# Kernel optimization log

Hardware: AMD Instinct MI355X
Metric: run time of the kernel (lower is better)

## Reference

```python
import jax, jax.numpy as jnp
import numpy as np

N_NODES = 100000
D_IN = 128
H_DIM = 128
N_EDGES = 1600000


def _gcn_conv(x, src, dst, dinv, W, b):
    # PyG GCNConv(improved=True): h = x @ W; out = A_hat h + b,
    # A_hat = D^{-1/2} (A + 2I) D^{-1/2}
    h = x @ W                                   # [N, H]
    norm = dinv[src] * dinv[dst]                # [E]
    agg = jnp.zeros_like(h).at[dst].add(h[src] * norm[:, None])
    agg = agg + h * (2.0 * dinv * dinv)[:, None]  # self-loop, weight 2.0
    return agg + b


def setup_inputs() -> dict:
    key = jax.random.key(0)
    ks = jax.random.split(key, 12)
    s = 1.0 / np.sqrt(D_IN)
    sh = 1.0 / np.sqrt(2 * H_DIM)
    inp = {
        "x": jax.random.normal(ks[0], (N_NODES, D_IN), jnp.float32),
        "edge_index": jax.random.randint(ks[1], (2, N_EDGES), 0, N_NODES, jnp.int64),
        # GCNConv weights (in -> hidden), bias
        "Wz": jax.random.uniform(ks[2], (D_IN, H_DIM), jnp.float32, -s, s),
        "bz": jnp.zeros((H_DIM,), jnp.float32),
        "Wr": jax.random.uniform(ks[3], (D_IN, H_DIM), jnp.float32, -s, s),
        "br": jnp.zeros((H_DIM,), jnp.float32),
        "Wh": jax.random.uniform(ks[4], (D_IN, H_DIM), jnp.float32, -s, s),
        "bh": jnp.zeros((H_DIM,), jnp.float32),
        # TGCN gate linears: Linear(2h, h)
        "lzW": jax.random.uniform(ks[5], (2 * H_DIM, H_DIM), jnp.float32, -sh, sh),
        "lzb": jax.random.uniform(ks[6], (H_DIM,), jnp.float32, -sh, sh),
        "lrW": jax.random.uniform(ks[7], (2 * H_DIM, H_DIM), jnp.float32, -sh, sh),
        "lrb": jax.random.uniform(ks[8], (H_DIM,), jnp.float32, -sh, sh),
        "lhW": jax.random.uniform(ks[9], (2 * H_DIM, H_DIM), jnp.float32, -sh, sh),
        "lhb": jax.random.uniform(ks[10], (H_DIM,), jnp.float32, -sh, sh),
        # final linear2: hidden -> 1
        "W2": jax.random.uniform(ks[11], (H_DIM, 1), jnp.float32, -1 / np.sqrt(H_DIM), 1 / np.sqrt(H_DIM)),
        "b2": jnp.zeros((1,), jnp.float32),
    }
    return inp


def reference(x, edge_index, Wz, bz, Wr, br, Wh, bh, lzW, lzb, lrW, lrb, lhW, lhb, W2, b2):
    src, dst = edge_index[0], edge_index[1]
    n = x.shape[0]
    # improved GCN norm: deg includes self-loop weight 2
    deg = jnp.zeros((n,), x.dtype).at[dst].add(jnp.ones_like(src, x.dtype)) + 2.0
    dinv = jnp.where(deg > 0, deg ** -0.5, 0.0)
    # TGCN cell with H0 = 0
    H0 = jnp.zeros((n, Wz.shape[1]), x.dtype)
    Z = jax.nn.sigmoid(jnp.concatenate([_gcn_conv(x, src, dst, dinv, Wz, bz), H0], axis=1) @ lzW + lzb)
    R = jax.nn.sigmoid(jnp.concatenate([_gcn_conv(x, src, dst, dinv, Wr, br), H0], axis=1) @ lrW + lrb)
    Ht = jnp.tanh(jnp.concatenate([_gcn_conv(x, src, dst, dinv, Wh, bh), H0 * R], axis=1) @ lhW + lhb)
    H = Z * H0 + (1.0 - Z) * Ht
    # forward: relu output is discarded (y = h overwrites), then linear2
    return H @ W2 + b2
```

## Files before the change

### kernel.cpp

```cpp
#include <hip/hip_runtime.h>
#include <math.h>

#define D 128
#define BSHIFT 9
#define CAP 12288
#define EPT 13
#define P1B 481
#define XCB 12500

typedef __attribute__((ext_vector_type(8))) short s8v;
typedef __attribute__((ext_vector_type(8))) unsigned short us8;
typedef __attribute__((ext_vector_type(4))) unsigned short us4;
typedef __attribute__((ext_vector_type(4))) float f4v;

__device__ __forceinline__ float bf2f(unsigned short u) {
    union { unsigned int i; float f; } v; v.i = ((unsigned int)u) << 16; return v.f;
}
__device__ __forceinline__ unsigned short f2bf(float f) {
    union { float f; unsigned int i; } v; v.f = f;
    unsigned int r = v.i + 0x7FFFu + ((v.i >> 16) & 1u);
    return (unsigned short)(r >> 16);
}

__global__ __launch_bounds__(256) void k_combo(
    const int* __restrict__ src, const int* __restrict__ dst, int E,
    int* __restrict__ bcur, unsigned int* __restrict__ pairs,
    const float* __restrict__ x, unsigned short* __restrict__ xb, int n4,
    const float* __restrict__ Wz, const float* __restrict__ bz,
    const float* __restrict__ lzW, const float* __restrict__ lzb,
    const float* __restrict__ Wh, const float* __restrict__ bh,
    const float* __restrict__ lhW, const float* __restrict__ lhb,
    unsigned short* __restrict__ Mt, float* __restrict__ c) {
    __shared__ int cnt[256];
    __shared__ int base[256];
    int bx = blockIdx.x, tid = threadIdx.x;

    if (bx < P1B) {
        unsigned int pk[EPT]; int rkbk[EPT];
        int e0 = bx * (EPT * 256) + tid;
        cnt[tid] = 0;
        __syncthreads();
        #pragma unroll
        for (int i = 0; i < EPT; ++i) {
            int e = e0 + i * 256;
            bool ok = e < E;
            int d = ok ? dst[e] : 0;
            int s = ok ? src[e] : 0;
            int bk = d >> BSHIFT;
            pk[i] = ((unsigned int)(d & ((1 << BSHIFT) - 1)) << 17) | (unsigned int)s;
            int r = ok ? atomicAdd(&cnt[bk], 1) : 0;
            rkbk[i] = (bk << 16) | r;
        }
        __syncthreads();
        if (cnt[tid] > 0) base[tid] = tid * CAP + atomicAdd(&bcur[tid], cnt[tid]);
        __syncthreads();
        #pragma unroll
        for (int i = 0; i < EPT; ++i) {
            int e = e0 + i * 256;
            if (e < E) {
                int bk = rkbk[i] >> 16;
                pairs[base[bk] + (rkbk[i] & 0xffff)] = pk[i];
            }
        }
    } else if (bx < P1B + XCB) {
        int i = (bx - P1B) * 256 + tid;
        if (i < n4) {
            float4 v = ((const float4*)x)[i];
            us4 o;
            o[0] = f2bf(v.x); o[1] = f2bf(v.y); o[2] = f2bf(v.z); o[3] = f2bf(v.w);
            ((us4*)xb)[i] = o;
        }
    } else {
        int k = bx - (P1B + XCB);
        int j = tid;
        int jj = j & 127;
        const float* W = (j < 128) ? Wz : Wh;
        const float* L = (j < 128) ? lzW : lhW;
        float s = 0.f;
        for (int t = 0; t < 128; ++t) s += W[k * 128 + t] * L[t * 128 + jj];
        Mt[(size_t)j * 128 + k] = f2bf(s);
        if (k == 0) {
            const float* b  = (j < 128) ? bz  : bh;
            const float* lb = (j < 128) ? lzb : lhb;
            float cs = lb[jj];
            for (int t = 0; t < 128; ++t) cs += b[t] * L[t * 128 + jj];
            c[j] = cs;
        }
    }
}

__global__ __launch_bounds__(256) void k_part2(const unsigned int* __restrict__ pairs,
                                               const int* __restrict__ bcur,
                                               int NB, int N, int E,
                                               int* __restrict__ rowptr,
                                               float* __restrict__ dinv,
                                               int* __restrict__ esrc) {
    __shared__ int cnt[512];
    __shared__ int lcur[512];
    __shared__ int ts[256];
    int b = blockIdx.x, tid = threadIdx.x;
    int n0 = b << BSHIFT;
    int nn = min(N - n0, 1 << BSHIFT);
    int tot = bcur[b];
    long pbase = (long)b * CAP;

    ts[tid] = (tid < b) ? bcur[tid] : 0;
    __syncthreads();
    for (int off = 128; off > 0; off >>= 1) {
        if (tid < off) ts[tid] += ts[tid + off];
        __syncthreads();
    }
    int obase = ts[0];
    __syncthreads();

    cnt[tid] = 0; cnt[tid + 256] = 0;
    __syncthreads();
    for (int i = tid; i < tot; i += 256)
        atomicAdd(&cnt[pairs[pbase + i] >> 17], 1);
    __syncthreads();

    int a0 = cnt[2 * tid], a1 = cnt[2 * tid + 1];
    int s = a0 + a1;
    ts[tid] = s; __syncthreads();
    for (int off = 1; off < 256; off <<= 1) {
        int add = (tid >= off) ? ts[tid - off] : 0;
        __syncthreads();
        ts[tid] += add;
        __syncthreads();
    }
    int excl = ts[tid] - s;
    lcur[2 * tid]     = obase + excl;
    lcur[2 * tid + 1] = obase + excl + a0;
    if (2 * tid < nn) {
        rowptr[n0 + 2 * tid] = obase + excl;
        dinv[n0 + 2 * tid]   = rsqrtf((float)a0 + 2.0f);
    }
    if (2 * tid + 1 < nn) {
        rowptr[n0 + 2 * tid + 1] = obase + excl + a0;
        dinv[n0 + 2 * tid + 1]   = rsqrtf((float)a1 + 2.0f);
    }
    if (b == 0 && tid == 0) rowptr[N] = E;
    __syncthreads();

    for (int i = tid; i < tot; i += 256) {
        unsigned int p = pairs[pbase + i];
        int dl = p >> 17;
        int pos = atomicAdd(&lcur[dl], 1);
        esrc[pos] = (int)(p & 0x1FFFFu);
    }
}

__global__ __launch_bounds__(256) void k_gather(const unsigned short* __restrict__ xb,
                                                const int* __restrict__ esrc,
                                                const int* __restrict__ rowptr,
                                                const float* __restrict__ dinv,
                                                unsigned short* __restrict__ xab, int N) {
    int node = (blockIdx.x * blockDim.x + threadIdx.x) >> 5;
    int sub  = threadIdx.x & 31;
    if (node >= N) return;
    int eo = sub >> 4, cs = sub & 15;
    int start = rowptr[node], end = rowptr[node + 1];
    float dd = dinv[node];
    float acc[8];
    #pragma unroll
    for (int j = 0; j < 8; ++j) acc[j] = 0.f;

    for (int base = start; base < end; base += 32) {
        int cnt = min(32, end - base);
        int myedge = 0; float mynorm = 0.f;
        if (sub < cnt) { myedge = esrc[base + sub]; mynorm = dinv[myedge]; }
        int pairs = (cnt + 1) >> 1;
        int i = 0;
        for (; i + 3 < pairs; i += 4) {
            int i0 = 2 * i + eo;
            int   s0 = __shfl(myedge, i0,     32); float w0 = __shfl(mynorm, i0,     32);
            int   s1 = __shfl(myedge, i0 + 2, 32); float w1 = __shfl(mynorm, i0 + 2, 32);
            int   s2 = __shfl(myedge, i0 + 4, 32); float w2 = __shfl(mynorm, i0 + 4, 32);
            int   s3 = __shfl(myedge, i0 + 6, 32); float w3 = __shfl(mynorm, i0 + 6, 32);
            us8 v0 = *(const us8*)(xb + (size_t)s0 * D + cs * 8);
            us8 v1 = *(const us8*)(xb + (size_t)s1 * D + cs * 8);
            us8 v2 = *(const us8*)(xb + (size_t)s2 * D + cs * 8);
            us8 v3 = *(const us8*)(xb + (size_t)s3 * D + cs * 8);
            #pragma unroll
            for (int j = 0; j < 8; ++j) acc[j] += bf2f(v0[j]) * w0;
            #pragma unroll
            for (int j = 0; j < 8; ++j) acc[j] += bf2f(v1[j]) * w1;
            #pragma unroll
            for (int j = 0; j < 8; ++j) acc[j] += bf2f(v2[j]) * w2;
            #pragma unroll
            for (int j = 0; j < 8; ++j) acc[j] += bf2f(v3[j]) * w3;
        }
        for (; i < pairs; ++i) {
            int i0 = 2 * i + eo;
            int   s0 = __shfl(myedge, i0, 32); float w0 = __shfl(mynorm, i0, 32);
            us8 v0 = *(const us8*)(xb + (size_t)s0 * D + cs * 8);
            #pragma unroll
            for (int j = 0; j < 8; ++j) acc[j] += bf2f(v0[j]) * w0;
        }
    }
    #pragma unroll
    for (int j = 0; j < 8; ++j) acc[j] += __shfl_xor(acc[j], 16);
    if (eo == 0) {
        us8 xs = *(const us8*)(xb + (size_t)node * D + cs * 8);
        float sfac = 2.f * dd * dd;
        us8 r;
        #pragma unroll
        for (int j = 0; j < 8; ++j) r[j] = f2bf(acc[j] * dd + bf2f(xs[j]) * sfac);
        *(us8*)(xab + (size_t)node * D + cs * 8) = r;
    }
}

#define ASTRIDE 136
__global__ __launch_bounds__(256, 4) void k_ep_mfma(
    const unsigned short* __restrict__ xab, const unsigned short* __restrict__ Mt,
    const float* __restrict__ c, const float* __restrict__ W2,
    const float* __restrict__ b2, float* __restrict__ out, int N) {
    __shared__ unsigned short Ast[64 * ASTRIDE];
    __shared__ float pbuf[4][64];

    int tid = threadIdx.x;
    int n0 = blockIdx.x * 64;
    int wv = tid >> 6;
    int lane = tid & 63;
    int l = lane & 15, q = lane >> 4;

    #pragma unroll
    for (int j = 0; j < 4; ++j) {
        int idx = tid + 256 * j;
        int row = idx >> 4, c16 = idx & 15;
        us8 v = {0, 0, 0, 0, 0, 0, 0, 0};
        if (n0 + row < N) v = *(const us8*)(xab + (size_t)(n0 + row) * D + c16 * 8);
        *(us8*)&Ast[row * ASTRIDE + c16 * 8] = v;
    }
    __syncthreads();

    int tz0 = 2 * wv;
    f4v acc[4][4];
    #pragma unroll
    for (int i = 0; i < 4; ++i)
        #pragma unroll
        for (int nt = 0; nt < 4; ++nt) acc[i][nt] = (f4v){0.f, 0.f, 0.f, 0.f};

    const unsigned short* Bb = Mt + (size_t)l * 128 + q * 8;

    #pragma unroll
    for (int ks = 0; ks < 4; ++ks) {
        s8v b[4];
        #pragma unroll
        for (int i = 0; i < 2; ++i) {
            b[i]     = *(const s8v*)(Bb + (size_t)(tz0 + i) * 16 * 128 + ks * 32);
            b[2 + i] = *(const s8v*)(Bb + (size_t)(8 + tz0 + i) * 16 * 128 + ks * 32);
        }
        #pragma unroll
        for (int nt = 0; nt < 4; ++nt) {
            s8v a = *(const s8v*)&Ast[(nt * 16 + l) * ASTRIDE + ks * 32 + q * 8];
            #pragma unroll
            for (int i = 0; i < 4; ++i)
                acc[i][nt] = __builtin_amdgcn_mfma_f32_16x16x32_bf16(a, b[i], acc[i][nt], 0, 0, 0);
        }
    }

    float p[4][4];
    #pragma unroll
    for (int nt = 0; nt < 4; ++nt)
        #pragma unroll
        for (int r = 0; r < 4; ++r) p[nt][r] = 0.f;
    #pragma unroll
    for (int i = 0; i < 2; ++i) {
        int col = (tz0 + i) * 16 + l;
        float cz = c[col], ch = c[128 + col], w2 = W2[col];
        #pragma unroll
        for (int nt = 0; nt < 4; ++nt)
            #pragma unroll
            for (int r = 0; r < 4; ++r) {
                float gz = acc[i][nt][r] + cz;
                float gh = acc[2 + i][nt][r] + ch;
                float z  = 1.f / (1.f + __expf(-gz));
                float ht = 1.f - 2.f / (__expf(2.f * gh) + 1.f);
                p[nt][r] += (1.f - z) * ht * w2;
            }
    }
    #pragma unroll
    for (int nt = 0; nt < 4; ++nt)
        #pragma unroll
        for (int r = 0; r < 4; ++r) {
            p[nt][r] += __shfl_xor(p[nt][r], 1);
            p[nt][r] += __shfl_xor(p[nt][r], 2);
            p[nt][r] += __shfl_xor(p[nt][r], 4);
            p[nt][r] += __shfl_xor(p[nt][r], 8);
        }
    if (l == 0) {
        #pragma unroll
        for (int nt = 0; nt < 4; ++nt)
            #pragma unroll
            for (int r = 0; r < 4; ++r)
                pbuf[wv][nt * 16 + q * 4 + r] = p[nt][r];
    }
    __syncthreads();
    if (tid < 64) {
        int n = n0 + tid;
        if (n < N)
            out[n] = pbuf[0][tid] + pbuf[1][tid] + pbuf[2][tid] + pbuf[3][tid] + b2[0];
    }
}

extern "C" void kernel_launch(void* const* d_in, const int* in_sizes, int n_in,
                              void* d_out, int out_size, void* d_ws, size_t ws_size,
                              hipStream_t stream) {
    const float* x    = (const float*)d_in[0];
    const int*   eidx = (const int*)d_in[1];
    const float* Wz   = (const float*)d_in[2];
    const float* bz   = (const float*)d_in[3];
    const float* Wh   = (const float*)d_in[6];
    const float* bh   = (const float*)d_in[7];
    const float* lzW  = (const float*)d_in[8];
    const float* lzb  = (const float*)d_in[9];
    const float* lhW  = (const float*)d_in[12];
    const float* lhb  = (const float*)d_in[13];
    const float* W2   = (const float*)d_in[14];
    const float* b2   = (const float*)d_in[15];
    float* out = (float*)d_out;

    int N = in_sizes[0] / D;
    int E = in_sizes[1] / 2;
    const int* src = eidx;
    const int* dst = eidx + E;
    int NB = (N + (1 << BSHIFT) - 1) >> BSHIFT;

    char* ws = (char*)d_ws;
    size_t off = 0;
    auto alloc = [&](size_t bytes) { void* p = ws + off; off += (bytes + 511) & ~(size_t)511; return p; };
    unsigned short* xb  = (unsigned short*)alloc((size_t)N * D * 2);
    unsigned short* xab = (unsigned short*)alloc((size_t)N * D * 2);
    int*   rowptr = (int*)  alloc((size_t)(N + 1) * 4);
    float* dinv   = (float*)alloc((size_t)N * 4);
    int*   esrc   = (int*)  alloc((size_t)E * 4);
    int*   bcur   = (int*)  alloc(256 * 4);
    unsigned short* Mt = (unsigned short*)alloc(256 * 128 * 2);
    float* c      = (float*)alloc(256 * 4);
    unsigned int* pairs = (unsigned int*)xab;

    hipMemsetAsync(bcur, 0, 256 * sizeof(int), stream);

    int n4 = N * (D / 4);
    k_combo<<<P1B + XCB + 128, 256, 0, stream>>>(
        src, dst, E, bcur, pairs, x, xb, n4,
        Wz, bz, lzW, lzb, Wh, bh, lhW, lhb, Mt, c);
    k_part2<<<NB, 256, 0, stream>>>(pairs, bcur, NB, N, E, rowptr, dinv, esrc);
    k_gather<<<(N * 32 + 255) / 256, 256, 0, stream>>>(xb, esrc, rowptr, dinv, xab, N);
    k_ep_mfma<<<(N + 63) / 64, 256, 0, stream>>>(xab, Mt, c, W2, b2, out, N);
}
```

Baseline: 251.6 us.

## Regroup preprocessing: bucket scatter alone, co-launch CSR build with conversion and weight fold

Edge bucketing now runs as a standalone kernel with 1024-thread blocks. The per-bucket CSR build, the x-to-bf16 conversion and the fused weight-matrix precompute are merged into a second kernel, also using 1024-thread blocks. This lets the bandwidth-heavy x conversion overlap the atomic-heavy CSR construction instead of the edge scatter. It also makes each bucket's block wider, in exchange for more idle threads in the scan phases and heavier shared-memory atomic contention per block.

```diff
diff --git a/kernel.cpp b/kernel.cpp
--- a/kernel.cpp
+++ b/kernel.cpp
@@ -4,9 +4,11 @@
 #define D 128
 #define BSHIFT 9
 #define CAP 12288
-#define EPT 13
-#define P1B 481
-#define XCB 12500
+#define EPT 7
+#define P1B 241
+#define P2B 196
+#define XCB2 3125
+#define PRB 32
 
 typedef __attribute__((ext_vector_type(8))) short s8v;
 typedef __attribute__((ext_vector_type(8))) unsigned short us8;
@@ -22,48 +24,117 @@
     return (unsigned short)(r >> 16);
 }
 
-__global__ __launch_bounds__(256) void k_combo(
+__global__ __launch_bounds__(1024) void k_part1(
     const int* __restrict__ src, const int* __restrict__ dst, int E,
-    int* __restrict__ bcur, unsigned int* __restrict__ pairs,
+    int* __restrict__ bcur, unsigned int* __restrict__ pairs) {
+    __shared__ int cnt[256];
+    __shared__ int base[256];
+    int bx = blockIdx.x, tid = threadIdx.x;
+
+    unsigned int pk[EPT]; int rkbk[EPT];
+    int e0 = bx * (EPT * 1024) + tid;
+    if (tid < 256) cnt[tid] = 0;
+    __syncthreads();
+    #pragma unroll
+    for (int i = 0; i < EPT; ++i) {
+        int e = e0 + i * 1024;
+        bool ok = e < E;
+        int d = ok ? dst[e] : 0;
+        int s = ok ? src[e] : 0;
+        int bk = d >> BSHIFT;
+        pk[i] = ((unsigned int)(d & ((1 << BSHIFT) - 1)) << 17) | (unsigned int)s;
+        int r = ok ? atomicAdd(&cnt[bk], 1) : 0;
+        rkbk[i] = (bk << 16) | r;
+    }
+    __syncthreads();
+    if (tid < 256 && cnt[tid] > 0)
+        base[tid] = tid * CAP + atomicAdd(&bcur[tid], cnt[tid]);
+    __syncthreads();
+    #pragma unroll
+    for (int i = 0; i < EPT; ++i) {
+        int e = e0 + i * 1024;
+        if (e < E) {
+            int bk = rkbk[i] >> 16;
+            pairs[base[bk] + (rkbk[i] & 0xffff)] = pk[i];
+        }
+    }
+}
+
+__global__ __launch_bounds__(1024) void k_mid(
+    const unsigned int* __restrict__ pairs, const int* __restrict__ bcur,
+    int N, int E,
+    int* __restrict__ rowptr, float* __restrict__ dinv, int* __restrict__ esrc,
     const float* __restrict__ x, unsigned short* __restrict__ xb, int n4,
     const float* __restrict__ Wz, const float* __restrict__ bz,
     const float* __restrict__ lzW, const float* __restrict__ lzb,
     const float* __restrict__ Wh, const float* __restrict__ bh,
     const float* __restrict__ lhW, const float* __restrict__ lhb,
     unsigned short* __restrict__ Mt, float* __restrict__ c) {
-    __shared__ int cnt[256];
-    __shared__ int base[256];
     int bx = blockIdx.x, tid = threadIdx.x;
 
-    if (bx < P1B) {
-        unsigned int pk[EPT]; int rkbk[EPT];
-        int e0 = bx * (EPT * 256) + tid;
-        cnt[tid] = 0;
-        __syncthreads();
-        #pragma unroll
-        for (int i = 0; i < EPT; ++i) {
-            int e = e0 + i * 256;
-            bool ok = e < E;
-            int d = ok ? dst[e] : 0;
-            int s = ok ? src[e] : 0;
-            int bk = d >> BSHIFT;
-            pk[i] = ((unsigned int)(d & ((1 << BSHIFT) - 1)) << 17) | (unsigned int)s;
-            int r = ok ? atomicAdd(&cnt[bk], 1) : 0;
-            rkbk[i] = (bk << 16) | r;
-        }
-        __syncthreads();
-        if (cnt[tid] > 0) base[tid] = tid * CAP + atomicAdd(&bcur[tid], cnt[tid]);
-        __syncthreads();
-        #pragma unroll
-        for (int i = 0; i < EPT; ++i) {
-            int e = e0 + i * 256;
-            if (e < E) {
-                int bk = rkbk[i] >> 16;
-                pairs[base[bk] + (rkbk[i] & 0xffff)] = pk[i];
+    if (bx < P2B) {
+        __shared__ int cnt[512];
+        __shared__ int lcur[512];
+        __shared__ int ts[256];
+        int b = bx;
+        int n0 = b << BSHIFT;
+        int nn = min(N - n0, 1 << BSHIFT);
+        int tot = bcur[b];
+        long pbase = (long)b * CAP;
+
+        if (tid < 256) ts[tid] = (tid < b) ? bcur[tid] : 0;
+        __syncthreads();
+        for (int off = 128; off > 0; off >>= 1) {
+            if (tid < off) ts[tid] += ts[tid + off];
+            __syncthreads();
+        }
+        int obase = ts[0];
+        __syncthreads();
+
+        if (tid < 512) cnt[tid] = 0;
+        __syncthreads();
+        for (int i = tid; i < tot; i += 1024)
+            atomicAdd(&cnt[pairs[pbase + i] >> 17], 1);
+        __syncthreads();
+
+        int a0 = 0, a1 = 0, s = 0;
+        if (tid < 256) {
+            a0 = cnt[2 * tid]; a1 = cnt[2 * tid + 1];
+            s = a0 + a1;
+            ts[tid] = s;
+        }
+        __syncthreads();
+        for (int off = 1; off < 256; off <<= 1) {
+            int add = 0;
+            if (tid < 256 && tid >= off) add = ts[tid - off];
+            __syncthreads();
+            if (tid < 256) ts[tid] += add;
+            __syncthreads();
+        }
+        if (tid < 256) {
+            int excl = ts[tid] - s;
+            lcur[2 * tid]     = obase + excl;
+            lcur[2 * tid + 1] = obase + excl + a0;
+            if (2 * tid < nn) {
+                rowptr[n0 + 2 * tid] = obase + excl;
+                dinv[n0 + 2 * tid]   = rsqrtf((float)a0 + 2.0f);
             }
-        }
-    } else if (bx < P1B + XCB) {
-        int i = (bx - P1B) * 256 + tid;
+            if (2 * tid + 1 < nn) {
+                rowptr[n0 + 2 * tid + 1] = obase + excl + a0;
+                dinv[n0 + 2 * tid + 1]   = rsqrtf((float)a1 + 2.0f);
+            }
+            if (b == 0 && tid == 0) rowptr[N] = E;
+        }
+        __syncthreads();
+
+        for (int i = tid; i < tot; i += 1024) {
+            unsigned int p = pairs[pbase + i];
+            int dl = p >> 17;
+            int pos = atomicAdd(&lcur[dl], 1);
+            esrc[pos] = (int)(p & 0x1FFFFu);
+        }
+    } else if (bx < P2B + XCB2) {
+        int i = (bx - P2B) * 1024 + tid;
         if (i < n4) {
             float4 v = ((const float4*)x)[i];
             us4 o;
@@ -71,8 +142,8 @@
             ((us4*)xb)[i] = o;
         }
     } else {
-        int k = bx - (P1B + XCB);
-        int j = tid;
+        int k = (bx - (P2B + XCB2)) * 4 + (tid >> 8);
+        int j = tid & 255;
         int jj = j & 127;
         const float* W = (j < 128) ? Wz : Wh;
         const float* L = (j < 128) ? lzW : lhW;
@@ -86,67 +157,6 @@
             for (int t = 0; t < 128; ++t) cs += b[t] * L[t * 128 + jj];
             c[j] = cs;
         }
-    }
-}
-
-__global__ __launch_bounds__(256) void k_part2(const unsigned int* __restrict__ pairs,
-                                               const int* __restrict__ bcur,
-                                               int NB, int N, int E,
-                                               int* __restrict__ rowptr,
-                                               float* __restrict__ dinv,
-                                               int* __restrict__ esrc) {
-    __shared__ int cnt[512];
-    __shared__ int lcur[512];
-    __shared__ int ts[256];
-    int b = blockIdx.x, tid = threadIdx.x;
-    int n0 = b << BSHIFT;
-    int nn = min(N - n0, 1 << BSHIFT);
-    int tot = bcur[b];
-    long pbase = (long)b * CAP;
-
-    ts[tid] = (tid < b) ? bcur[tid] : 0;
-    __syncthreads();
-    for (int off = 128; off > 0; off >>= 1) {
-        if (tid < off) ts[tid] += ts[tid + off];
-        __syncthreads();
-    }
-    int obase = ts[0];
-    __syncthreads();
-
-    cnt[tid] = 0; cnt[tid + 256] = 0;
-    __syncthreads();
-    for (int i = tid; i < tot; i += 256)
-        atomicAdd(&cnt[pairs[pbase + i] >> 17], 1);
-    __syncthreads();
-
-    int a0 = cnt[2 * tid], a1 = cnt[2 * tid + 1];
-    int s = a0 + a1;
-    ts[tid] = s; __syncthreads();
-    for (int off = 1; off < 256; off <<= 1) {
-        int add = (tid >= off) ? ts[tid - off] : 0;
-        __syncthreads();
-        ts[tid] += add;
-        __syncthreads();
-    }
-    int excl = ts[tid] - s;
-    lcur[2 * tid]     = obase + excl;
-    lcur[2 * tid + 1] = obase + excl + a0;
-    if (2 * tid < nn) {
-        rowptr[n0 + 2 * tid] = obase + excl;
-        dinv[n0 + 2 * tid]   = rsqrtf((float)a0 + 2.0f);
-    }
-    if (2 * tid + 1 < nn) {
-        rowptr[n0 + 2 * tid + 1] = obase + excl + a0;
-        dinv[n0 + 2 * tid + 1]   = rsqrtf((float)a1 + 2.0f);
-    }
-    if (b == 0 && tid == 0) rowptr[N] = E;
-    __syncthreads();
-
-    for (int i = tid; i < tot; i += 256) {
-        unsigned int p = pairs[pbase + i];
-        int dl = p >> 17;
-        int pos = atomicAdd(&lcur[dl], 1);
-        esrc[pos] = (int)(p & 0x1FFFFu);
     }
 }
 
@@ -325,7 +335,6 @@
     int E = in_sizes[1] / 2;
     const int* src = eidx;
     const int* dst = eidx + E;
-    int NB = (N + (1 << BSHIFT) - 1) >> BSHIFT;
 
     char* ws = (char*)d_ws;
     size_t off = 0;
@@ -343,10 +352,10 @@
     hipMemsetAsync(bcur, 0, 256 * sizeof(int), stream);
 
     int n4 = N * (D / 4);
-    k_combo<<<P1B + XCB + 128, 256, 0, stream>>>(
-        src, dst, E, bcur, pairs, x, xb, n4,
-        Wz, bz, lzW, lzb, Wh, bh, lhW, lhb, Mt, c);
-    k_part2<<<NB, 256, 0, stream>>>(pairs, bcur, NB, N, E, rowptr, dinv, esrc);
+    k_part1<<<P1B, 1024, 0, stream>>>(src, dst, E, bcur, pairs);
+    k_mid<<<P2B + XCB2 + PRB, 1024, 0, stream>>>(
+        pairs, bcur, N, E, rowptr, dinv, esrc,
+        x, xb, n4, Wz, bz, lzW, lzb, Wh, bh, lhW, lhb, Mt, c);
     k_gather<<<(N * 32 + 255) / 256, 256, 0, stream>>>(xb, esrc, rowptr, dinv, xab, N);
     k_ep_mfma<<<(N + 63) / 64, 256, 0, stream>>>(xab, Mt, c, W2, b2, out, N);
 }
```

New measurement: 244.3 us. 2.9% less time.
